# Performance work log

Hardware: AMD Instinct MI355X
Metric: run time of the kernel (lower is better)

Reference implementation:

```python
import jax, jax.numpy as jnp
import numpy as np

TEMP = 1.0
EULER_GAMMA = 0.5772156649015329
BIG = 1.0e9


def setup_inputs() -> dict:
    key = jax.random.key(0)
    k = jax.random.split(key, 8)
    B, N, D, H = 32, 1024, 1024, 512  # batch, seq, d_model, hidden_size//2
    queries = jax.random.normal(k[0], (B, N, D), jnp.float32)
    queries_mask = jnp.ones((B, N), dtype=bool)
    W1 = jax.random.normal(k[1], (D, H), jnp.float32) * 0.02
    b1 = jnp.zeros((H,), jnp.float32)
    W2 = jax.random.normal(k[2], (H, 1), jnp.float32) * 0.02
    b2 = jnp.zeros((1,), jnp.float32)
    uniform_noise = jax.random.uniform(k[3], (B, N, 1), jnp.float32, 0.0, 1e-5)
    gumbel_noise = jax.random.gumbel(k[4], (B, N, 1), jnp.float32)
    return {"queries": queries, "queries_mask": queries_mask, "W1": W1, "b1": b1,
            "W2": W2, "b2": b2, "uniform_noise": uniform_noise,
            "gumbel_noise": gumbel_noise, "action_refinement": 1}


def reference(queries, queries_mask, W1, b1, W2, b2, uniform_noise, gumbel_noise, action_refinement):
    B, N, D = queries.shape
    # block0: Dense(H, relu) -> Dense(1); then softplus clamp + log + tiny uniform noise
    h = jax.nn.relu(jnp.einsum('bnd,dh->bnh', queries, W1) + b1)
    acts = jnp.einsum('bnh,ho->bno', h, W2) + b2                      # [B,N,1]
    acts = jnp.log(jnp.maximum(jax.nn.softplus(acts), 1e-5)) + uniform_noise
    acts = jnp.repeat(acts, action_refinement, axis=0)                # [BR,N,1]
    vmask = jnp.repeat(queries_mask[:, None, :].astype(jnp.float32), action_refinement, axis=0)  # [BR,1,N]
    n_valid = jnp.sum(vmask, axis=-1)                                 # [BR,1]
    mask_n1 = jnp.transpose(vmask, (0, 2, 1))                         # [BR,N,1]
    sqz_mask = mask_n1[..., 0]                                        # [BR,N]
    masked_acts = jnp.where(mask_n1 > 0, acts, -1e6)                  # [BR,N,1]
    perturb = masked_acts + gumbel_noise                              # [BR,N,1]
    # deterministic NeuralSort
    s = (jnp.exp(perturb) * mask_n1)[..., 0]                          # [BR,N]
    A = jnp.abs(s[:, :, None] - s[:, None, :])                        # [BR,N,N]
    Bmat = jnp.sum(A, axis=-1, keepdims=True)                         # A @ (1 1^T): row sums broadcast
    scaling = (N + 1 - 2 * (jnp.arange(N) + 1)).astype(jnp.float32)   # [N]
    C = s[:, :, None] * scaling[None, None, :]                        # [BR,N,N]
    P_hat = jnp.transpose(C - Bmat, (0, 2, 1)) - (1.0 - vmask) * BIG  # [BR,N,N]
    # greedy argmax permutation extraction (find_permu), vectorized over batch
    BR = P_hat.shape[0]
    def step(flag, row):                                              # row: [BR,N]
        tmp = row - flag * BIG
        idx = jnp.argmax(tmp, axis=-1)
        flag = jnp.maximum(flag, jax.nn.one_hot(idx, N, dtype=flag.dtype))
        return flag, idx
    _, idxs = jax.lax.scan(step, jnp.zeros((BR, N), jnp.float32), jnp.transpose(P_hat, (1, 0, 2)))
    chosen = jnp.transpose(idxs).astype(jnp.int32)                    # [BR,N]
    chosen = jnp.concatenate([jnp.zeros((BR, 1), jnp.int32), chosen[:, :-1]], axis=-1)
    id_permu = jnp.arange(N, dtype=jnp.int32)[None, :]
    permu = jnp.where(sqz_mask > 0, chosen, id_permu)                 # [BR,N]
    sample_permu = jax.nn.one_hot(permu, N, axis=-1, dtype=jnp.float32)
    # Plackett-Luce log-likelihood of sampled permutation
    exp_actis = jnp.exp(jnp.take_along_axis(masked_acts[..., 0], permu, axis=-1))
    rev_cumsum = jnp.cumsum(exp_actis[:, ::-1], axis=-1)[:, ::-1]
    eps = 1e-20
    log_nom = (jnp.log(exp_actis + eps) - jnp.log(rev_cumsum + eps)) * sqz_mask
    log_nom = jnp.sum(log_nom, axis=-1, keepdims=True)                # [BR,1]
    log_norm = jnp.zeros_like(log_nom)
    # KL term
    sqz_acts = acts[..., 0]
    kl1 = n_valid * (np.log(TEMP) - 1.0 + EULER_GAMMA * (1.0 / TEMP - 1.0))
    s1 = (1.0 / TEMP) * jnp.sum(sqz_acts * sqz_mask, axis=-1).reshape(-1, 1)
    s2 = jnp.sum(jnp.exp(-1.0 / TEMP * jnp.maximum(sqz_acts * sqz_mask, -20.0 * TEMP)), axis=-1).reshape(-1, 1) - (jnp.float32(N) - n_valid)
    kl = kl1 + s1 + s2 * jnp.exp(jax.lax.lgamma(jnp.float32(1.0 + 1.0 / TEMP)))
    return sample_permu, masked_acts[..., 0], kl, log_nom, log_norm
```

## Files before the change

### kernel.cpp

```cpp
#include <hip/hip_runtime.h>
#include <math.h>

#define BB 32
#define NN 1024
#define DD 1024
#define HH 512

#define OUT0_OFF 0
#define OUT1_OFF (BB * NN * NN)
#define OUT2_OFF (OUT1_OFF + BB * NN)
#define OUT3_OFF (OUT2_OFF + BB)
#define OUT4_OFF (OUT3_OFF + BB)

#define WS_ACTS 0
#define WS_W1T  131072
#define WS_RANK 1179648

typedef __attribute__((ext_vector_type(8))) short short8;
typedef __attribute__((ext_vector_type(4))) float floatx4;

__device__ inline unsigned int f2bf(float x) {
    unsigned int u = __builtin_bit_cast(unsigned int, x);
    return (u + 0x7FFFu + ((u >> 16) & 1u)) >> 16;
}

__global__ __launch_bounds__(1024) void w1t_kernel(const float* __restrict__ W1,
                                                   unsigned short* __restrict__ W1T)
{
    __shared__ float T[32][33];
    const int tx = threadIdx.x, ty = threadIdx.y;
    const int d0 = blockIdx.x * 32, h0 = blockIdx.y * 32;
    T[ty][tx] = W1[(d0 + ty) * HH + h0 + tx];
    __syncthreads();
    W1T[(size_t)(h0 + ty) * DD + d0 + tx] = (unsigned short)f2bf(T[tx][ty]);
}

__global__ __launch_bounds__(256, 2) void gemm_acts_kernel(
    const float* __restrict__ q, const unsigned short* __restrict__ W1T,
    const float* __restrict__ b1, const float* __restrict__ W2,
    const float* __restrict__ b2, const float* __restrict__ unoise,
    float* __restrict__ acts_ws, float* __restrict__ out1)
{
    __shared__ float red[64][4];

    const int tid = threadIdx.x;
    const int w = tid >> 6, lane = tid & 63;
    const int c = lane & 15, qd = lane >> 4;
    const int m0 = blockIdx.x * 64;

    floatx4 acc[8][4];
    #pragma unroll
    for (int tn = 0; tn < 8; ++tn)
        #pragma unroll
        for (int tm = 0; tm < 4; ++tm)
            acc[tn][tm] = (floatx4){0.f, 0.f, 0.f, 0.f};

    const float* aqb = q + (size_t)(m0 + c) * DD + qd * 8;
    const unsigned short* bb = W1T + (size_t)(w * 128 + c) * DD + qd * 8;

    float4 araw[4][2];
    #pragma unroll
    for (int tm = 0; tm < 4; ++tm) {
        const float* ap = aqb + (size_t)tm * 16 * DD;
        araw[tm][0] = *(const float4*)(ap);
        araw[tm][1] = *(const float4*)(ap + 4);
    }

    #pragma unroll 1
    for (int kk = 0; kk < 32; ++kk) {
        uint4 bq[8];
        #pragma unroll
        for (int tn = 0; tn < 8; ++tn)
            bq[tn] = *(const uint4*)(bb + (size_t)tn * 16 * DD + kk * 32);

        short8 af[4];
        #pragma unroll
        for (int tm = 0; tm < 4; ++tm) {
            float4 v0 = araw[tm][0], v1 = araw[tm][1];
            uint4 u;
            u.x = f2bf(v0.x) | (f2bf(v0.y) << 16);
            u.y = f2bf(v0.z) | (f2bf(v0.w) << 16);
            u.z = f2bf(v1.x) | (f2bf(v1.y) << 16);
            u.w = f2bf(v1.z) | (f2bf(v1.w) << 16);
            af[tm] = __builtin_bit_cast(short8, u);
        }

        if (kk < 31) {
            #pragma unroll
            for (int tm = 0; tm < 4; ++tm) {
                const float* ap = aqb + (size_t)tm * 16 * DD + (kk + 1) * 32;
                araw[tm][0] = *(const float4*)(ap);
                araw[tm][1] = *(const float4*)(ap + 4);
            }
        }

        #pragma unroll
        for (int tn = 0; tn < 8; ++tn) {
            short8 bf = __builtin_bit_cast(short8, bq[tn]);
            #pragma unroll
            for (int tm = 0; tm < 4; ++tm)
                acc[tn][tm] = __builtin_amdgcn_mfma_f32_16x16x32_bf16(
                    af[tm], bf, acc[tn][tm], 0, 0, 0);
        }
    }

    float b1v[8], w2v[8];
    #pragma unroll
    for (int tn = 0; tn < 8; ++tn) {
        int col = w * 128 + tn * 16 + c;
        b1v[tn] = b1[col];
        w2v[tn] = W2[col];
    }
    #pragma unroll
    for (int tm = 0; tm < 4; ++tm) {
        #pragma unroll
        for (int r = 0; r < 4; ++r) {
            float p = 0.f;
            #pragma unroll
            for (int tn = 0; tn < 8; ++tn) {
                float v = acc[tn][tm][r] + b1v[tn];
                p = fmaf(fmaxf(v, 0.f), w2v[tn], p);
            }
            p += __shfl_xor(p, 1);
            p += __shfl_xor(p, 2);
            p += __shfl_xor(p, 4);
            p += __shfl_xor(p, 8);
            if (c == 0) red[tm * 16 + qd * 4 + r][w] = p;
        }
    }
    __syncthreads();
    if (tid < 64) {
        float raw = red[tid][0] + red[tid][1] + red[tid][2] + red[tid][3] + b2[0];
        float sp = fmaxf(raw, 0.f) + log1pf(expf(-fabsf(raw)));
        int row = m0 + tid;
        float av = logf(fmaxf(sp, 1e-5f)) + unoise[row];
        acts_ws[row] = av;
        out1[row]    = av;
    }
}

__global__ __launch_bounds__(256) void rank_kernel(
    const float* __restrict__ acts_ws, const float* __restrict__ gumbel,
    int* __restrict__ rank)
{
    __shared__ float P[NN];
    const int b = blockIdx.x >> 2;
    const int chunk = blockIdx.x & 3;
    const int tid = threadIdx.x;
    #pragma unroll
    for (int r = 0; r < 4; ++r) {
        int j = r * 256 + tid;
        P[j] = acts_ws[b * NN + j] + gumbel[b * NN + j];
    }
    __syncthreads();
    const int i = chunk * 256 + tid;
    const float pert = P[i];
    int cnt = 0;
    const float4* P4 = (const float4*)P;
    for (int j4 = 0; j4 < NN / 4; ++j4) {
        float4 pv = P4[j4];
        int j = j4 * 4;
        cnt += (pv.x > pert) || (pv.x == pert && j + 0 < i);
        cnt += (pv.y > pert) || (pv.y == pert && j + 1 < i);
        cnt += (pv.z > pert) || (pv.z == pert && j + 2 < i);
        cnt += (pv.w > pert) || (pv.w == pert && j + 3 < i);
    }
    rank[b * NN + i] = cnt;
}

__global__ __launch_bounds__(1024) void permu_stats_kernel(
    const float* __restrict__ acts_ws, int* __restrict__ rank_perm,
    float* __restrict__ out2, float* __restrict__ out3, float* __restrict__ out4)
{
    __shared__ float A[NN];
    __shared__ int   IDX[NN];
    __shared__ float WT[16];
    __shared__ float RS[48];

    const int b = blockIdx.x, i = threadIdx.x;
    const int lane = i & 63, w = i >> 6;

    float a = acts_ws[b * NN + i];
    A[i] = a;
    IDX[rank_perm[b * NN + i]] = i;
    __syncthreads();

    int perm = (i == 0) ? 0 : IDX[i - 1];
    rank_perm[b * NN + i] = perm;

    float e = expf(A[perm]);

    float s = e;
    #pragma unroll
    for (int off = 1; off < 64; off <<= 1) {
        float v = __shfl_down(s, off);
        if (lane + off < 64) s += v;
    }
    if (lane == 0) WT[w] = s;
    __syncthreads();
    float suff = 0.f;
    for (int ww = w + 1; ww < 16; ++ww) suff += WT[ww];
    float S = s + suff;
    float term = logf(e + 1e-20f) - logf(S + 1e-20f);

    float r0 = term, r1 = a, r2 = expf(-fmaxf(a, -20.f));
    #pragma unroll
    for (int off = 32; off > 0; off >>= 1) {
        r0 += __shfl_down(r0, off);
        r1 += __shfl_down(r1, off);
        r2 += __shfl_down(r2, off);
    }
    if (lane == 0) { RS[w] = r0; RS[16 + w] = r1; RS[32 + w] = r2; }
    __syncthreads();
    if (i == 0) {
        float t0 = 0.f, t1 = 0.f, t2 = 0.f;
        for (int ww = 0; ww < 16; ++ww) {
            t0 += RS[ww]; t1 += RS[16 + ww]; t2 += RS[32 + ww];
        }
        out2[b] = -(float)NN + t1 + t2;
        out3[b] = t0;
        out4[b] = 0.f;
    }
}

__global__ __launch_bounds__(256) void onehot_kernel(
    const int* __restrict__ perm, float4* __restrict__ out0)
{
    const int t = threadIdx.x;
    const size_t row0 = (size_t)blockIdx.x * 16;
    #pragma unroll
    for (int r = 0; r < 16; ++r) {
        int p = perm[row0 + r];
        float on = ((p >> 2) == t) ? 1.0f : 0.0f;
        float4 v;
        v.x = ((p & 3) == 0) ? on : 0.0f;
        v.y = ((p & 3) == 1) ? on : 0.0f;
        v.z = ((p & 3) == 2) ? on : 0.0f;
        v.w = ((p & 3) == 3) ? on : 0.0f;
        out0[(row0 + r) * 256 + t] = v;
    }
}

extern "C" void kernel_launch(void* const* d_in, const int* in_sizes, int n_in,
                              void* d_out, int out_size, void* d_ws, size_t ws_size,
                              hipStream_t stream)
{
    const float* q      = (const float*)d_in[0];
    const float* W1     = (const float*)d_in[2];
    const float* b1     = (const float*)d_in[3];
    const float* W2     = (const float*)d_in[4];
    const float* b2     = (const float*)d_in[5];
    const float* unoise = (const float*)d_in[6];
    const float* gumbel = (const float*)d_in[7];

    float* out = (float*)d_out;
    char*  ws  = (char*)d_ws;
    float*          acts = (float*)(ws + WS_ACTS);
    unsigned short* W1T  = (unsigned short*)(ws + WS_W1T);
    int*            rkpm = (int*)(ws + WS_RANK);

    w1t_kernel<<<dim3(32, 16), dim3(32, 32), 0, stream>>>(W1, W1T);
    gemm_acts_kernel<<<(BB * NN) / 64, 256, 0, stream>>>(q, W1T, b1, W2, b2,
                                                         unoise, acts,
                                                         out + OUT1_OFF);
    rank_kernel<<<BB * 4, 256, 0, stream>>>(acts, gumbel, rkpm);
    permu_stats_kernel<<<BB, 1024, 0, stream>>>(acts, rkpm, out + OUT2_OFF,
                                                out + OUT3_OFF, out + OUT4_OFF);
    onehot_kernel<<<2048, 256, 0, stream>>>(rkpm, (float4*)(out + OUT0_OFF));
}
```

Before: 369.7 us.

## Pre-convert queries to bf16, split GEMM over hidden halves, double-buffer loads

Adds a pass that converts the whole fp32 query tensor to bf16, staging it in the unused one-hot output buffer, so the GEMM reads half the bytes and skips per-iteration conversion. The GEMM is split into two blocks per row tile, each covering half of the hidden columns, which doubles the grid and halves accumulator registers. It also uses explicit register double-buffering of A/B fragments. Partial sums are combined in a new finalize kernel. The trade-off is an extra full read and write of the 128MB input plus two extra launches, and duplicated A reads across the two halves.

```diff
diff --git a/kernel.cpp b/kernel.cpp
--- a/kernel.cpp
+++ b/kernel.cpp
@@ -15,6 +15,7 @@
 #define WS_ACTS 0
 #define WS_W1T  131072
 #define WS_RANK 1179648
+#define WS_PART 1310720
 
 typedef __attribute__((ext_vector_type(8))) short short8;
 typedef __attribute__((ext_vector_type(4))) float floatx4;
@@ -22,6 +23,24 @@
 __device__ inline unsigned int f2bf(float x) {
     unsigned int u = __builtin_bit_cast(unsigned int, x);
     return (u + 0x7FFFu + ((u >> 16) & 1u)) >> 16;
+}
+
+__global__ __launch_bounds__(256) void convert_q_kernel(
+    const float* __restrict__ q, uint4* __restrict__ qb)
+{
+    int idx = blockIdx.x * blockDim.x + threadIdx.x;
+    int stride = gridDim.x * blockDim.x;
+    const float4* q4 = (const float4*)q;
+    const int n8 = BB * NN * DD / 8;
+    for (int i = idx; i < n8; i += stride) {
+        float4 v0 = q4[2 * i], v1 = q4[2 * i + 1];
+        uint4 u;
+        u.x = f2bf(v0.x) | (f2bf(v0.y) << 16);
+        u.y = f2bf(v0.z) | (f2bf(v0.w) << 16);
+        u.z = f2bf(v1.x) | (f2bf(v1.y) << 16);
+        u.w = f2bf(v1.z) | (f2bf(v1.w) << 16);
+        qb[i] = u;
+    }
 }
 
 __global__ __launch_bounds__(1024) void w1t_kernel(const float* __restrict__ W1,
@@ -35,79 +54,76 @@
     W1T[(size_t)(h0 + ty) * DD + d0 + tx] = (unsigned short)f2bf(T[tx][ty]);
 }
 
+__device__ __forceinline__ void load_group(const uint4* __restrict__ aub,
+                                           const uint4* __restrict__ bub, int g,
+                                           uint4 (&ab)[4][2], uint4 (&bb)[4][2])
+{
+    #pragma unroll
+    for (int t = 0; t < 4; ++t) {
+        #pragma unroll
+        for (int k2 = 0; k2 < 2; ++k2) {
+            ab[t][k2] = aub[t * 2048 + (g * 2 + k2) * 4];
+            bb[t][k2] = bub[t * 2048 + (g * 2 + k2) * 4];
+        }
+    }
+}
+
+__device__ __forceinline__ void compute_group(const uint4 (&ab)[4][2],
+                                              const uint4 (&bb)[4][2],
+                                              floatx4 (&acc)[4][4])
+{
+    #pragma unroll
+    for (int k2 = 0; k2 < 2; ++k2) {
+        #pragma unroll
+        for (int tn = 0; tn < 4; ++tn) {
+            short8 bf = __builtin_bit_cast(short8, bb[tn][k2]);
+            #pragma unroll
+            for (int tm = 0; tm < 4; ++tm)
+                acc[tn][tm] = __builtin_amdgcn_mfma_f32_16x16x32_bf16(
+                    __builtin_bit_cast(short8, ab[tm][k2]), bf, acc[tn][tm], 0, 0, 0);
+        }
+    }
+}
+
 __global__ __launch_bounds__(256, 2) void gemm_acts_kernel(
-    const float* __restrict__ q, const unsigned short* __restrict__ W1T,
+    const unsigned short* __restrict__ qb, const unsigned short* __restrict__ W1T,
     const float* __restrict__ b1, const float* __restrict__ W2,
-    const float* __restrict__ b2, const float* __restrict__ unoise,
-    float* __restrict__ acts_ws, float* __restrict__ out1)
+    float* __restrict__ part)
 {
     __shared__ float red[64][4];
 
     const int tid = threadIdx.x;
     const int w = tid >> 6, lane = tid & 63;
     const int c = lane & 15, qd = lane >> 4;
-    const int m0 = blockIdx.x * 64;
-
-    floatx4 acc[8][4];
-    #pragma unroll
-    for (int tn = 0; tn < 8; ++tn)
+    const int m0 = (blockIdx.x >> 1) * 64;
+    const int half = blockIdx.x & 1;
+    const int ncol0 = half * 256 + w * 64;
+
+    floatx4 acc[4][4];
+    #pragma unroll
+    for (int tn = 0; tn < 4; ++tn)
         #pragma unroll
         for (int tm = 0; tm < 4; ++tm)
             acc[tn][tm] = (floatx4){0.f, 0.f, 0.f, 0.f};
 
-    const float* aqb = q + (size_t)(m0 + c) * DD + qd * 8;
-    const unsigned short* bb = W1T + (size_t)(w * 128 + c) * DD + qd * 8;
-
-    float4 araw[4][2];
-    #pragma unroll
-    for (int tm = 0; tm < 4; ++tm) {
-        const float* ap = aqb + (size_t)tm * 16 * DD;
-        araw[tm][0] = *(const float4*)(ap);
-        araw[tm][1] = *(const float4*)(ap + 4);
-    }
+    const uint4* aub = (const uint4*)qb + (size_t)(m0 + c) * 128 + qd;
+    const uint4* bub = (const uint4*)W1T + (size_t)(ncol0 + c) * 128 + qd;
+
+    uint4 a0[4][2], b0[4][2], a1[4][2], bq1[4][2];
+    load_group(aub, bub, 0, a0, b0);
 
     #pragma unroll 1
-    for (int kk = 0; kk < 32; ++kk) {
-        uint4 bq[8];
-        #pragma unroll
-        for (int tn = 0; tn < 8; ++tn)
-            bq[tn] = *(const uint4*)(bb + (size_t)tn * 16 * DD + kk * 32);
-
-        short8 af[4];
-        #pragma unroll
-        for (int tm = 0; tm < 4; ++tm) {
-            float4 v0 = araw[tm][0], v1 = araw[tm][1];
-            uint4 u;
-            u.x = f2bf(v0.x) | (f2bf(v0.y) << 16);
-            u.y = f2bf(v0.z) | (f2bf(v0.w) << 16);
-            u.z = f2bf(v1.x) | (f2bf(v1.y) << 16);
-            u.w = f2bf(v1.z) | (f2bf(v1.w) << 16);
-            af[tm] = __builtin_bit_cast(short8, u);
-        }
-
-        if (kk < 31) {
-            #pragma unroll
-            for (int tm = 0; tm < 4; ++tm) {
-                const float* ap = aqb + (size_t)tm * 16 * DD + (kk + 1) * 32;
-                araw[tm][0] = *(const float4*)(ap);
-                araw[tm][1] = *(const float4*)(ap + 4);
-            }
-        }
-
-        #pragma unroll
-        for (int tn = 0; tn < 8; ++tn) {
-            short8 bf = __builtin_bit_cast(short8, bq[tn]);
-            #pragma unroll
-            for (int tm = 0; tm < 4; ++tm)
-                acc[tn][tm] = __builtin_amdgcn_mfma_f32_16x16x32_bf16(
-                    af[tm], bf, acc[tn][tm], 0, 0, 0);
-        }
-    }
-
-    float b1v[8], w2v[8];
-    #pragma unroll
-    for (int tn = 0; tn < 8; ++tn) {
-        int col = w * 128 + tn * 16 + c;
+    for (int g = 0; g < 16; g += 2) {
+        load_group(aub, bub, g + 1, a1, bq1);
+        compute_group(a0, b0, acc);
+        if (g + 2 < 16) load_group(aub, bub, g + 2, a0, b0);
+        compute_group(a1, bq1, acc);
+    }
+
+    float b1v[4], w2v[4];
+    #pragma unroll
+    for (int tn = 0; tn < 4; ++tn) {
+        int col = ncol0 + tn * 16 + c;
         b1v[tn] = b1[col];
         w2v[tn] = W2[col];
     }
@@ -117,7 +133,7 @@
         for (int r = 0; r < 4; ++r) {
             float p = 0.f;
             #pragma unroll
-            for (int tn = 0; tn < 8; ++tn) {
+            for (int tn = 0; tn < 4; ++tn) {
                 float v = acc[tn][tm][r] + b1v[tn];
                 p = fmaf(fmaxf(v, 0.f), w2v[tn], p);
             }
@@ -129,14 +145,22 @@
         }
     }
     __syncthreads();
-    if (tid < 64) {
-        float raw = red[tid][0] + red[tid][1] + red[tid][2] + red[tid][3] + b2[0];
-        float sp = fmaxf(raw, 0.f) + log1pf(expf(-fabsf(raw)));
-        int row = m0 + tid;
-        float av = logf(fmaxf(sp, 1e-5f)) + unoise[row];
-        acts_ws[row] = av;
-        out1[row]    = av;
-    }
+    if (tid < 64)
+        part[(size_t)half * (BB * NN) + m0 + tid] =
+            red[tid][0] + red[tid][1] + red[tid][2] + red[tid][3];
+}
+
+__global__ __launch_bounds__(256) void finalize_acts_kernel(
+    const float* __restrict__ part, const float* __restrict__ b2,
+    const float* __restrict__ unoise, float* __restrict__ acts_ws,
+    float* __restrict__ out1)
+{
+    int r = blockIdx.x * 256 + threadIdx.x;
+    float raw = part[r] + part[BB * NN + r] + b2[0];
+    float sp = fmaxf(raw, 0.f) + log1pf(expf(-fabsf(raw)));
+    float av = logf(fmaxf(sp, 1e-5f)) + unoise[r];
+    acts_ws[r] = av;
+    out1[r]    = av;
 }
 
 __global__ __launch_bounds__(256) void rank_kernel(
@@ -258,11 +282,14 @@
     float*          acts = (float*)(ws + WS_ACTS);
     unsigned short* W1T  = (unsigned short*)(ws + WS_W1T);
     int*            rkpm = (int*)(ws + WS_RANK);
-
+    float*          part = (float*)(ws + WS_PART);
+    unsigned short* qb   = (unsigned short*)(out + OUT0_OFF);
+
+    convert_q_kernel<<<2048, 256, 0, stream>>>(q, (uint4*)qb);
     w1t_kernel<<<dim3(32, 16), dim3(32, 32), 0, stream>>>(W1, W1T);
-    gemm_acts_kernel<<<(BB * NN) / 64, 256, 0, stream>>>(q, W1T, b1, W2, b2,
-                                                         unoise, acts,
-                                                         out + OUT1_OFF);
+    gemm_acts_kernel<<<(BB * NN / 64) * 2, 256, 0, stream>>>(qb, W1T, b1, W2, part);
+    finalize_acts_kernel<<<BB * NN / 256, 256, 0, stream>>>(part, b2, unoise,
+                                                            acts, out + OUT1_OFF);
     rank_kernel<<<BB * 4, 256, 0, stream>>>(acts, gumbel, rkpm);
     permu_stats_kernel<<<BB, 1024, 0, stream>>>(acts, rkpm, out + OUT2_OFF,
                                                 out + OUT3_OFF, out + OUT4_OFF);
```

New measurement: 411.7 us. 1.11x slower.

## Pre-convert queries to bf16, tile GEMM through LDS, fuse rank into stats

Applied to the files above, without the earlier changes.

Adds a prep kernel that converts the fp32 queries to bf16 and stores them in the not-yet-written one-hot output buffer. The same kernel also transposes W1. The GEMM becomes a 128x128 tiled kernel that stages A and B through swizzled LDS with async global-to-LDS loads and splits H into four chunks, each writing its partial W2 dot products. A fused stats kernel then sums the partials, applies softplus/log, computes ranks and does the permutation stats. The aim is better data reuse and fewer launches, at the cost of an extra full read and write of queries plus scratch use of the output buffer.

```diff
diff --git a/kernel.cpp b/kernel.cpp
--- a/kernel.cpp
+++ b/kernel.cpp
@@ -12,9 +12,11 @@
 #define OUT3_OFF (OUT2_OFF + BB)
 #define OUT4_OFF (OUT3_OFF + BB)
 
-#define WS_ACTS 0
 #define WS_W1T  131072
 #define WS_RANK 1179648
+
+#define QB_FOFF   0
+#define PART_FOFF (24 * 1024 * 1024)
 
 typedef __attribute__((ext_vector_type(8))) short short8;
 typedef __attribute__((ext_vector_type(4))) float floatx4;
@@ -24,90 +26,112 @@
     return (u + 0x7FFFu + ((u >> 16) & 1u)) >> 16;
 }
 
-__global__ __launch_bounds__(1024) void w1t_kernel(const float* __restrict__ W1,
-                                                   unsigned short* __restrict__ W1T)
+__device__ __forceinline__ void async16(const unsigned short* g, short* l) {
+    __builtin_amdgcn_global_load_lds(
+        (const __attribute__((address_space(1))) unsigned int*)g,
+        (__attribute__((address_space(3))) unsigned int*)l, 16, 0, 0);
+}
+
+__global__ __launch_bounds__(256) void prep_kernel(
+    const float* __restrict__ q, uint4* __restrict__ qb,
+    const float* __restrict__ W1, unsigned short* __restrict__ W1T)
 {
     __shared__ float T[32][33];
-    const int tx = threadIdx.x, ty = threadIdx.y;
-    const int d0 = blockIdx.x * 32, h0 = blockIdx.y * 32;
-    T[ty][tx] = W1[(d0 + ty) * HH + h0 + tx];
-    __syncthreads();
-    W1T[(size_t)(h0 + ty) * DD + d0 + tx] = (unsigned short)f2bf(T[tx][ty]);
-}
-
-__global__ __launch_bounds__(256, 2) void gemm_acts_kernel(
-    const float* __restrict__ q, const unsigned short* __restrict__ W1T,
-    const float* __restrict__ b1, const float* __restrict__ W2,
-    const float* __restrict__ b2, const float* __restrict__ unoise,
-    float* __restrict__ acts_ws, float* __restrict__ out1)
-{
-    __shared__ float red[64][4];
-
-    const int tid = threadIdx.x;
-    const int w = tid >> 6, lane = tid & 63;
-    const int c = lane & 15, qd = lane >> 4;
-    const int m0 = blockIdx.x * 64;
-
-    floatx4 acc[8][4];
-    #pragma unroll
-    for (int tn = 0; tn < 8; ++tn)
-        #pragma unroll
-        for (int tm = 0; tm < 4; ++tm)
-            acc[tn][tm] = (floatx4){0.f, 0.f, 0.f, 0.f};
-
-    const float* aqb = q + (size_t)(m0 + c) * DD + qd * 8;
-    const unsigned short* bb = W1T + (size_t)(w * 128 + c) * DD + qd * 8;
-
-    float4 araw[4][2];
-    #pragma unroll
-    for (int tm = 0; tm < 4; ++tm) {
-        const float* ap = aqb + (size_t)tm * 16 * DD;
-        araw[tm][0] = *(const float4*)(ap);
-        araw[tm][1] = *(const float4*)(ap + 4);
-    }
-
-    #pragma unroll 1
-    for (int kk = 0; kk < 32; ++kk) {
-        uint4 bq[8];
-        #pragma unroll
-        for (int tn = 0; tn < 8; ++tn)
-            bq[tn] = *(const uint4*)(bb + (size_t)tn * 16 * DD + kk * 32);
-
-        short8 af[4];
-        #pragma unroll
-        for (int tm = 0; tm < 4; ++tm) {
-            float4 v0 = araw[tm][0], v1 = araw[tm][1];
+    if (blockIdx.x < 2048) {
+        int idx = blockIdx.x * 256 + threadIdx.x;
+        const float4* q4 = (const float4*)q;
+        const int n8 = BB * NN * DD / 8;
+        for (int i = idx; i < n8; i += 2048 * 256) {
+            float4 v0 = q4[2 * i], v1 = q4[2 * i + 1];
             uint4 u;
             u.x = f2bf(v0.x) | (f2bf(v0.y) << 16);
             u.y = f2bf(v0.z) | (f2bf(v0.w) << 16);
             u.z = f2bf(v1.x) | (f2bf(v1.y) << 16);
             u.w = f2bf(v1.z) | (f2bf(v1.w) << 16);
-            af[tm] = __builtin_bit_cast(short8, u);
-        }
-
-        if (kk < 31) {
+            qb[i] = u;
+        }
+    } else {
+        int bid = blockIdx.x - 2048;
+        int d0 = (bid & 31) * 32, h0 = (bid >> 5) * 32;
+        int tx = threadIdx.x & 31, ty0 = threadIdx.x >> 5;
+        #pragma unroll
+        for (int r = 0; r < 4; ++r) {
+            int ty = ty0 * 4 + r;
+            T[ty][tx] = W1[(d0 + ty) * HH + h0 + tx];
+        }
+        __syncthreads();
+        #pragma unroll
+        for (int r = 0; r < 4; ++r) {
+            int ty = ty0 * 4 + r;
+            W1T[(size_t)(h0 + ty) * DD + d0 + tx] = (unsigned short)f2bf(T[tx][ty]);
+        }
+    }
+}
+
+__global__ __launch_bounds__(256, 3) void gemm_acts_kernel(
+    const unsigned short* __restrict__ qb, const unsigned short* __restrict__ W1T,
+    const float* __restrict__ b1, const float* __restrict__ W2,
+    float* __restrict__ part)
+{
+    __shared__ short As[128 * 64];
+    __shared__ short Bs[128 * 64];
+    __shared__ float red[128][2];
+
+    const int tid = threadIdx.x;
+    const int w = tid >> 6, l = tid & 63;
+    const int c = l & 15, qd = l >> 4;
+    const int wm = w & 1, wn = w >> 1;
+    const int nchunk = blockIdx.x & 3;
+    const int m0 = (blockIdx.x >> 2) * 128;
+    const int n0 = nchunk * 128;
+
+    floatx4 acc[4][4];
+    #pragma unroll
+    for (int tn = 0; tn < 4; ++tn)
+        #pragma unroll
+        for (int tm = 0; tm < 4; ++tm)
+            acc[tn][tm] = (floatx4){0.f, 0.f, 0.f, 0.f};
+
+    const int srow = w * 8 + (l >> 3);
+    const int scs  = (l & 7) ^ ((l >> 3) & 7);
+    const unsigned short* aG = qb  + (size_t)(m0 + srow) * DD + scs * 8;
+    const unsigned short* bG = W1T + (size_t)(n0 + srow) * DD + scs * 8;
+
+    for (int kk = 0; kk < 16; ++kk) {
+        const int ko = kk * 64;
+        #pragma unroll
+        for (int i = 0; i < 4; ++i) {
+            async16(aG + (size_t)(i * 32) * DD + ko, &As[i * 2048 + w * 512]);
+            async16(bG + (size_t)(i * 32) * DD + ko, &Bs[i * 2048 + w * 512]);
+        }
+        __syncthreads();
+        #pragma unroll
+        for (int h = 0; h < 2; ++h) {
+            short8 af[4], bfr[4];
             #pragma unroll
             for (int tm = 0; tm < 4; ++tm) {
-                const float* ap = aqb + (size_t)tm * 16 * DD + (kk + 1) * 32;
-                araw[tm][0] = *(const float4*)(ap);
-                araw[tm][1] = *(const float4*)(ap + 4);
+                int r = wm * 64 + tm * 16 + c;
+                af[tm] = *(const short8*)&As[r * 64 + ((h * 4 + qd) ^ (r & 7)) * 8];
             }
-        }
-
-        #pragma unroll
-        for (int tn = 0; tn < 8; ++tn) {
-            short8 bf = __builtin_bit_cast(short8, bq[tn]);
-            #pragma unroll
-            for (int tm = 0; tm < 4; ++tm)
-                acc[tn][tm] = __builtin_amdgcn_mfma_f32_16x16x32_bf16(
-                    af[tm], bf, acc[tn][tm], 0, 0, 0);
-        }
-    }
-
-    float b1v[8], w2v[8];
-    #pragma unroll
-    for (int tn = 0; tn < 8; ++tn) {
-        int col = w * 128 + tn * 16 + c;
+            #pragma unroll
+            for (int tn = 0; tn < 4; ++tn) {
+                int r = wn * 64 + tn * 16 + c;
+                bfr[tn] = *(const short8*)&Bs[r * 64 + ((h * 4 + qd) ^ (r & 7)) * 8];
+            }
+            #pragma unroll
+            for (int tn = 0; tn < 4; ++tn)
+                #pragma unroll
+                for (int tm = 0; tm < 4; ++tm)
+                    acc[tn][tm] = __builtin_amdgcn_mfma_f32_16x16x32_bf16(
+                        af[tm], bfr[tn], acc[tn][tm], 0, 0, 0);
+        }
+        __syncthreads();
+    }
+
+    float b1v[4], w2v[4];
+    #pragma unroll
+    for (int tn = 0; tn < 4; ++tn) {
+        int col = n0 + wn * 64 + tn * 16 + c;
         b1v[tn] = b1[col];
         w2v[tn] = W2[col];
     }
@@ -117,7 +141,7 @@
         for (int r = 0; r < 4; ++r) {
             float p = 0.f;
             #pragma unroll
-            for (int tn = 0; tn < 8; ++tn) {
+            for (int tn = 0; tn < 4; ++tn) {
                 float v = acc[tn][tm][r] + b1v[tn];
                 p = fmaf(fmaxf(v, 0.f), w2v[tn], p);
             }
@@ -125,35 +149,39 @@
             p += __shfl_xor(p, 2);
             p += __shfl_xor(p, 4);
             p += __shfl_xor(p, 8);
-            if (c == 0) red[tm * 16 + qd * 4 + r][w] = p;
-        }
-    }
-    __syncthreads();
-    if (tid < 64) {
-        float raw = red[tid][0] + red[tid][1] + red[tid][2] + red[tid][3] + b2[0];
-        float sp = fmaxf(raw, 0.f) + log1pf(expf(-fabsf(raw)));
-        int row = m0 + tid;
-        float av = logf(fmaxf(sp, 1e-5f)) + unoise[row];
-        acts_ws[row] = av;
-        out1[row]    = av;
-    }
-}
-
-__global__ __launch_bounds__(256) void rank_kernel(
-    const float* __restrict__ acts_ws, const float* __restrict__ gumbel,
-    int* __restrict__ rank)
-{
+            if (c == 0) red[wm * 64 + tm * 16 + qd * 4 + r][wn] = p;
+        }
+    }
+    __syncthreads();
+    if (tid < 128)
+        part[(size_t)nchunk * (BB * NN) + m0 + tid] = red[tid][0] + red[tid][1];
+}
+
+__global__ __launch_bounds__(1024) void stats_kernel(
+    const float* __restrict__ part, const float* __restrict__ b2,
+    const float* __restrict__ unoise, const float* __restrict__ gumbel,
+    int* __restrict__ rkpm, float* __restrict__ out1,
+    float* __restrict__ out2, float* __restrict__ out3, float* __restrict__ out4)
+{
+    __shared__ float A[NN];
     __shared__ float P[NN];
-    const int b = blockIdx.x >> 2;
-    const int chunk = blockIdx.x & 3;
-    const int tid = threadIdx.x;
-    #pragma unroll
-    for (int r = 0; r < 4; ++r) {
-        int j = r * 256 + tid;
-        P[j] = acts_ws[b * NN + j] + gumbel[b * NN + j];
-    }
-    __syncthreads();
-    const int i = chunk * 256 + tid;
+    __shared__ int   IDX[NN];
+    __shared__ float WT[16];
+    __shared__ float RS[48];
+
+    const int b = blockIdx.x, i = threadIdx.x;
+    const int lane = i & 63, w = i >> 6;
+    const int gi = b * NN + i;
+
+    float raw = part[gi] + part[BB * NN + gi] + part[2 * BB * NN + gi] +
+                part[3 * BB * NN + gi] + b2[0];
+    float sp = fmaxf(raw, 0.f) + log1pf(expf(-fabsf(raw)));
+    float a = logf(fmaxf(sp, 1e-5f)) + unoise[gi];
+    out1[gi] = a;
+    A[i] = a;
+    P[i] = a + gumbel[gi];
+    __syncthreads();
+
     const float pert = P[i];
     int cnt = 0;
     const float4* P4 = (const float4*)P;
@@ -165,28 +193,11 @@
         cnt += (pv.z > pert) || (pv.z == pert && j + 2 < i);
         cnt += (pv.w > pert) || (pv.w == pert && j + 3 < i);
     }
-    rank[b * NN + i] = cnt;
-}
-
-__global__ __launch_bounds__(1024) void permu_stats_kernel(
-    const float* __restrict__ acts_ws, int* __restrict__ rank_perm,
-    float* __restrict__ out2, float* __restrict__ out3, float* __restrict__ out4)
-{
-    __shared__ float A[NN];
-    __shared__ int   IDX[NN];
-    __shared__ float WT[16];
-    __shared__ float RS[48];
-
-    const int b = blockIdx.x, i = threadIdx.x;
-    const int lane = i & 63, w = i >> 6;
-
-    float a = acts_ws[b * NN + i];
-    A[i] = a;
-    IDX[rank_perm[b * NN + i]] = i;
+    IDX[cnt] = i;
     __syncthreads();
 
     int perm = (i == 0) ? 0 : IDX[i - 1];
-    rank_perm[b * NN + i] = perm;
+    rkpm[gi] = perm;
 
     float e = expf(A[perm]);
 
@@ -255,16 +266,15 @@
 
     float* out = (float*)d_out;
     char*  ws  = (char*)d_ws;
-    float*          acts = (float*)(ws + WS_ACTS);
     unsigned short* W1T  = (unsigned short*)(ws + WS_W1T);
     int*            rkpm = (int*)(ws + WS_RANK);
-
-    w1t_kernel<<<dim3(32, 16), dim3(32, 32), 0, stream>>>(W1, W1T);
-    gemm_acts_kernel<<<(BB * NN) / 64, 256, 0, stream>>>(q, W1T, b1, W2, b2,
-                                                         unoise, acts,
-                                                         out + OUT1_OFF);
-    rank_kernel<<<BB * 4, 256, 0, stream>>>(acts, gumbel, rkpm);
-    permu_stats_kernel<<<BB, 1024, 0, stream>>>(acts, rkpm, out + OUT2_OFF,
-                                                out + OUT3_OFF, out + OUT4_OFF);
+    unsigned short* qb   = (unsigned short*)(out + OUT0_OFF + QB_FOFF);
+    float*          part = out + OUT0_OFF + PART_FOFF;
+
+    prep_kernel<<<2560, 256, 0, stream>>>(q, (uint4*)qb, W1, W1T);
+    gemm_acts_kernel<<<(BB * NN / 128) * 4, 256, 0, stream>>>(qb, W1T, b1, W2, part);
+    stats_kernel<<<BB, 1024, 0, stream>>>(part, b2, unoise, gumbel, rkpm,
+                                          out + OUT1_OFF, out + OUT2_OFF,
+                                          out + OUT3_OFF, out + OUT4_OFF);
     onehot_kernel<<<2048, 256, 0, stream>>>(rkpm, (float4*)(out + OUT0_OFF));
 }
```

Measured after the change: 344.1 us. -6.9%, faster.
